# Kernel tuning notes

Hardware: AMD Instinct MI355X
Metric: run time of the kernel (lower is better)

The kernel has to match this reference:

```python
import jax, jax.numpy as jnp
import numpy as np

HIDDEN = 2048
N_HEADS = 16
HEAD_DIM = HIDDEN // N_HEADS
BATCH = 2
SEQ = 2048
N_CP = max(8, int(HIDDEN * HIDDEN / 128.9))  # 32540 control points


def _spline_to_weight(cp, out_dim, in_dim):
    # Reconstruct full weight matrix by sampling the control-point curve at
    # out_dim*in_dim evenly spaced parameter values (piecewise-linear spline eval).
    n = cp.shape[0]
    t = jnp.linspace(0.0, 1.0, out_dim * in_dim)
    xp = jnp.linspace(0.0, 1.0, n)
    return jnp.interp(t, xp, cp).reshape(out_dim, in_dim)


def setup_inputs() -> dict:
    key = jax.random.key(0)
    ks = jax.random.split(key, 5)
    hidden_states = jax.random.normal(ks[0], (BATCH, SEQ, HIDDEN), dtype=jnp.float32)
    cp_q = jax.random.normal(ks[1], (N_CP,), dtype=jnp.float32) * 0.02
    cp_k = jax.random.normal(ks[2], (N_CP,), dtype=jnp.float32) * 0.02
    cp_v = jax.random.normal(ks[3], (N_CP,), dtype=jnp.float32) * 0.02
    cp_o = jax.random.normal(ks[4], (N_CP,), dtype=jnp.float32) * 0.02
    # additive causal mask [1,1,S,S]
    causal = jnp.tril(jnp.ones((SEQ, SEQ), dtype=bool))
    attention_mask = jnp.where(causal, 0.0, -1e9).astype(jnp.float32)[None, None]
    return {
        'hidden_states': hidden_states,
        'cp_q': cp_q, 'cp_k': cp_k, 'cp_v': cp_v, 'cp_o': cp_o,
        'attention_mask': attention_mask,
    }


def reference(hidden_states, cp_q, cp_k, cp_v, cp_o, attention_mask):
    B, S, H = hidden_states.shape
    q_w = _spline_to_weight(cp_q, H, H)
    k_w = _spline_to_weight(cp_k, H, H)
    v_w = _spline_to_weight(cp_v, H, H)
    o_w = _spline_to_weight(cp_o, H, H)

    # F.linear(x, W) == x @ W.T
    q = (hidden_states @ q_w.T).reshape(B, S, N_HEADS, HEAD_DIM).transpose(0, 2, 1, 3)
    k = (hidden_states @ k_w.T).reshape(B, S, N_HEADS, HEAD_DIM).transpose(0, 2, 1, 3)
    v = (hidden_states @ v_w.T).reshape(B, S, N_HEADS, HEAD_DIM).transpose(0, 2, 1, 3)

    scale = 1.0 / np.sqrt(HEAD_DIM).astype(np.float32)
    scores = jnp.einsum('bhqd,bhkd->bhqk', q, k) * scale + attention_mask
    probs = jax.nn.softmax(scores.astype(jnp.float32), axis=-1).astype(q.dtype)
    attn = jnp.einsum('bhqk,bhkd->bhqd', probs, v)
    attn = attn.transpose(0, 2, 1, 3).reshape(B, S, H)
    return attn @ o_w.T
```

## Files before the change

kernel.cpp:

```cpp
#include <hip/hip_runtime.h>
#include <stdint.h>

typedef unsigned short u16;
typedef __bf16 bf16x8 __attribute__((ext_vector_type(8)));
typedef float f32x4 __attribute__((ext_vector_type(4)));
typedef u16 u16x4 __attribute__((ext_vector_type(4)));

#define MFMA16(a, b, c) __builtin_amdgcn_mfma_f32_16x16x32_bf16((a), (b), (c), 0, 0, 0)

__device__ __forceinline__ u16 f2bf(float f) {
  uint32_t u = __builtin_bit_cast(uint32_t, f);
  u += 0x7FFFu + ((u >> 16) & 1u);
  return (u16)(u >> 16);
}
__device__ __forceinline__ bf16x8 cvt8(f32x4 lo, f32x4 hi) {
  union { u16 u[8]; bf16x8 v; } r;
#pragma unroll
  for (int j = 0; j < 4; j++) { r.u[j] = f2bf(lo[j]); r.u[4 + j] = f2bf(hi[j]); }
  return r.v;
}
__device__ __forceinline__ void gld_lds16(const void* g, void* l) {
  __builtin_amdgcn_global_load_lds(
      (const __attribute__((address_space(1))) uint32_t*)g,
      (__attribute__((address_space(3))) uint32_t*)l, 16, 0, 0);
}

__global__ void spline_kernel(const float* __restrict__ cpq, const float* __restrict__ cpk,
                              const float* __restrict__ cpv, const float* __restrict__ cpo,
                              u16* __restrict__ Wqkv, u16* __restrict__ Wo,
                              int n, double factor) {
  int idx = blockIdx.x * 256 + threadIdx.x;
  int w = idx >> 22;
  int i = idx & 4194303;
  const float* cp = (w == 0) ? cpq : (w == 1) ? cpk : (w == 2) ? cpv : cpo;
  double u = (double)i * factor;
  int i0 = (int)u;
  if (i0 > n - 2) i0 = n - 2;
  float fr = (float)(u - (double)i0);
  float f0 = cp[i0], f1 = cp[i0 + 1];
  u16 bv = f2bf(f0 + fr * (f1 - f0));
  if (w < 3) Wqkv[idx] = bv; else Wo[i] = bv;
}

__global__ void cvt_kernel(const float* __restrict__ x, u16* __restrict__ xb) {
  size_t i = ((size_t)blockIdx.x * 256 + threadIdx.x) * 8;
  const f32x4* p = (const f32x4*)(x + i);
  *(bf16x8*)(xb + i) = cvt8(p[0], p[1]);
}

template <int MODE>
__global__ __launch_bounds__(256, 2)
void gemm_bt(const u16* __restrict__ A, const u16* __restrict__ B,
             u16* __restrict__ oQ, u16* __restrict__ oK, u16* __restrict__ oV,
             float* __restrict__ oC) {
  constexpr int KD = 2048;
  __shared__ __align__(16) u16 As[128 * 64];
  __shared__ __align__(16) u16 Bs[128 * 64];
  const int tid = threadIdx.x;
  const int wave = tid >> 6, lane = tid & 63, quad = lane >> 4, l16 = lane & 15;
  const int wm = wave & 1, wn = wave >> 1;
  const int m0 = blockIdx.y * 128, n0 = blockIdx.x * 128;

  size_t aoff[4], boff[4];
  int lslot[4];
#pragma unroll
  for (int b = 0; b < 4; b++) {
    int s = wave * 256 + b * 64 + lane;
    int r = s >> 3, c = s & 7, gc = c ^ (r & 7);
    lslot[b] = s * 16;
    aoff[b] = (size_t)(m0 + r) * (KD * 2) + gc * 16;
    boff[b] = (size_t)(n0 + r) * (KD * 2) + gc * 16;
  }
  const char* Ab = (const char*)A;
  const char* Bb = (const char*)B;
  char* AsB = (char*)As;
  char* BsB = (char*)Bs;

  f32x4 acc[4][4];
  const f32x4 fz = {0.f, 0.f, 0.f, 0.f};
#pragma unroll
  for (int i = 0; i < 4; i++)
#pragma unroll
    for (int j = 0; j < 4; j++) acc[i][j] = fz;

  for (int kt = 0; kt < KD / 64; ++kt) {
    if (kt) __syncthreads();
#pragma unroll
    for (int b = 0; b < 4; b++) {
      gld_lds16(Ab + aoff[b], AsB + lslot[b]);
      gld_lds16(Bb + boff[b], BsB + lslot[b]);
      aoff[b] += 128;
      boff[b] += 128;
    }
    __syncthreads();
#pragma unroll
    for (int t = 0; t < 2; t++) {
      bf16x8 af[4], bfb[4];
#pragma unroll
      for (int i = 0; i < 4; i++) {
        int row = wm * 64 + i * 16 + l16;
        int ch = (t * 4 + quad) ^ (row & 7);
        af[i] = *(const bf16x8*)(AsB + row * 128 + ch * 16);
      }
#pragma unroll
      for (int j = 0; j < 4; j++) {
        int row = wn * 64 + j * 16 + l16;
        int ch = (t * 4 + quad) ^ (row & 7);
        bfb[j] = *(const bf16x8*)(BsB + row * 128 + ch * 16);
      }
#pragma unroll
      for (int i = 0; i < 4; i++)
#pragma unroll
        for (int j = 0; j < 4; j++) acc[i][j] = MFMA16(af[i], bfb[j], acc[i][j]);
    }
  }

  if (MODE == 0) {
#pragma unroll
    for (int j = 0; j < 4; j++) {
      int nb = n0 + wn * 64 + j * 16;
      int sel = nb >> 11;
      int h = (nb >> 7) & 15;
      int d = (nb & 127) + l16;
#pragma unroll
      for (int i = 0; i < 4; i++) {
        int mrow = m0 + wm * 64 + i * 16 + quad * 4;
        int bq = mrow >> 11, srow = mrow & 2047;
        if (sel == 2) {
          u16x4 pk = {f2bf(acc[i][j][0]), f2bf(acc[i][j][1]),
                      f2bf(acc[i][j][2]), f2bf(acc[i][j][3])};
          *(u16x4*)&oV[(size_t)(((bq << 4) + h) * 128 + d) * 2048 + srow] = pk;
        } else {
          u16* dst = (sel == 0) ? oQ : oK;
          int base = ((bq << 4) + h) * 2048;
#pragma unroll
          for (int r = 0; r < 4; r++)
            dst[(size_t)(base + srow + r) * 128 + d] = f2bf(acc[i][j][r]);
        }
      }
    }
  } else {
#pragma unroll
    for (int j = 0; j < 4; j++) {
      int col = n0 + wn * 64 + j * 16 + l16;
#pragma unroll
      for (int i = 0; i < 4; i++) {
        int mrow = m0 + wm * 64 + i * 16 + quad * 4;
#pragma unroll
        for (int r = 0; r < 4; r++) oC[(size_t)(mrow + r) * 2048 + col] = acc[i][j][r];
      }
    }
  }
}

__global__ __launch_bounds__(256, 2)
void flash_attn(const u16* __restrict__ Q, const u16* __restrict__ Kg,
                const u16* __restrict__ Vt, u16* __restrict__ attn) {
  __shared__ __align__(16) u16 Ks[64 * 128];
  __shared__ __align__(16) u16 Vs[128 * 64];
  __shared__ __align__(16) u16 Ps[128 * 72];
  const int tid = threadIdx.x;
  const int wave = tid >> 6, lane = tid & 63, quad = lane >> 4, l16 = lane & 15;
  const int L = blockIdx.x;
  const int bh = L & 31;
  const int qi = (L >> 5) & 7;
  const int qt = (L >= 256) ? (15 - qi) : qi;
  const int q0 = qt * 128;
  const u16* Qb = Q + (size_t)bh * 2048 * 128;
  const u16* Kb = Kg + (size_t)bh * 2048 * 128;
  const u16* Vb = Vt + (size_t)bh * 128 * 2048;

  bf16x8 qf[2][4];
#pragma unroll
  for (int i = 0; i < 2; i++) {
    int row = q0 + wave * 32 + i * 16 + l16;
#pragma unroll
    for (int t = 0; t < 4; t++)
      qf[i][t] = *(const bf16x8*)(Qb + (size_t)row * 128 + t * 32 + quad * 8);
  }

  f32x4 o_acc[2][8];
  const f32x4 fz = {0.f, 0.f, 0.f, 0.f};
#pragma unroll
  for (int i = 0; i < 2; i++)
#pragma unroll
    for (int j = 0; j < 8; j++) o_acc[i][j] = fz;
  float m_i[2][4], l_i[2][4];
#pragma unroll
  for (int i = 0; i < 2; i++)
#pragma unroll
    for (int r = 0; r < 4; r++) { m_i[i][r] = -1e30f; l_i[i][r] = 0.f; }

  int koff[4], voff[4], lslot[4];
#pragma unroll
  for (int b = 0; b < 4; b++) {
    int s = wave * 256 + b * 64 + lane;
    lslot[b] = s * 16;
    {
      int r = s >> 4, c = s & 15;
      int gc = (c & 8) | ((c & 7) ^ (r & 7));
      koff[b] = r * 256 + gc * 16;
    }
    {
      int r = s >> 3, c = s & 7;
      int gc = c ^ (r & 7);
      voff[b] = r * 4096 + gc * 16;
    }
  }
  const char* KbB = (const char*)Kb;
  const char* VbB = (const char*)Vb;
  char* KsB = (char*)Ks;
  char* VsB = (char*)Vs;

  const int ktmax = 2 * qt + 1;
  const float scale = 0.08838834764831845f;

  for (int kt = 0; kt <= ktmax; ++kt) {
    const int k0 = kt * 64;
    if (kt) __syncthreads();
#pragma unroll
    for (int b = 0; b < 4; b++) {
      gld_lds16(KbB + (size_t)k0 * 256 + koff[b], KsB + lslot[b]);
      gld_lds16(VbB + (size_t)k0 * 2 + voff[b], VsB + lslot[b]);
    }
    __syncthreads();

    f32x4 sacc[2][4];
#pragma unroll
    for (int i = 0; i < 2; i++)
#pragma unroll
      for (int j = 0; j < 4; j++) sacc[i][j] = fz;
#pragma unroll
    for (int j = 0; j < 4; j++) {
      int rowb = j * 16 + l16;
#pragma unroll
      for (int t = 0; t < 4; t++) {
        int cc = t * 4 + quad;
        int ch = (cc & 8) | ((cc & 7) ^ (rowb & 7));
        bf16x8 bfr = *(const bf16x8*)(KsB + rowb * 256 + ch * 16);
        sacc[0][j] = MFMA16(qf[0][t], bfr, sacc[0][j]);
        sacc[1][j] = MFMA16(qf[1][t], bfr, sacc[1][j]);
      }
    }

    const bool do_mask = (kt >= 2 * qt);
#pragma unroll
    for (int i = 0; i < 2; i++) {
      const int rbase = q0 + wave * 32 + i * 16 + quad * 4;
#pragma unroll
      for (int r = 0; r < 4; r++) {
        float mloc = -1e30f;
#pragma unroll
        for (int j = 0; j < 4; j++) {
          float v = sacc[i][j][r] * scale;
          if (do_mask && (k0 + j * 16 + l16 > rbase + r)) v = -1e30f;
          sacc[i][j][r] = v;
          mloc = fmaxf(mloc, v);
        }
        mloc = fmaxf(mloc, __shfl_xor(mloc, 1, 16));
        mloc = fmaxf(mloc, __shfl_xor(mloc, 2, 16));
        mloc = fmaxf(mloc, __shfl_xor(mloc, 4, 16));
        mloc = fmaxf(mloc, __shfl_xor(mloc, 8, 16));
        float mold = m_i[i][r];
        float mnew = fmaxf(mold, mloc);
        float alpha = __expf(mold - mnew);
        m_i[i][r] = mnew;
        float rs = 0.f;
#pragma unroll
        for (int j = 0; j < 4; j++) {
          float p = __expf(sacc[i][j][r] - mnew);
          sacc[i][j][r] = p;
          rs += p;
        }
        rs += __shfl_xor(rs, 1, 16);
        rs += __shfl_xor(rs, 2, 16);
        rs += __shfl_xor(rs, 4, 16);
        rs += __shfl_xor(rs, 8, 16);
        l_i[i][r] = alpha * l_i[i][r] + rs;
#pragma unroll
        for (int j = 0; j < 8; j++) o_acc[i][j][r] *= alpha;
      }
#pragma unroll
      for (int r = 0; r < 4; r++) {
        int prow = wave * 32 + i * 16 + quad * 4 + r;
#pragma unroll
        for (int j = 0; j < 4; j++) Ps[prow * 72 + j * 16 + l16] = f2bf(sacc[i][j][r]);
      }
    }
    __syncthreads();

#pragma unroll
    for (int t = 0; t < 2; t++) {
      bf16x8 af0 = *(const bf16x8*)((char*)Ps + (wave * 32 + l16) * 144 + (t * 32 + quad * 8) * 2);
      bf16x8 af1 = *(const bf16x8*)((char*)Ps + (wave * 32 + 16 + l16) * 144 + (t * 32 + quad * 8) * 2);
#pragma unroll
      for (int j = 0; j < 8; j++) {
        int vrow = j * 16 + l16;
        int ch = (t * 4 + quad) ^ (vrow & 7);
        bf16x8 bfr = *(const bf16x8*)(VsB + vrow * 128 + ch * 16);
        o_acc[0][j] = MFMA16(af0, bfr, o_acc[0][j]);
        o_acc[1][j] = MFMA16(af1, bfr, o_acc[1][j]);
      }
    }
  }

  const int bb = bh >> 4, h = bh & 15;
#pragma unroll
  for (int i = 0; i < 2; i++) {
#pragma unroll
    for (int r = 0; r < 4; r++) {
      float inv = 1.f / l_i[i][r];
      int srow = q0 + wave * 32 + i * 16 + quad * 4 + r;
      size_t base = ((size_t)(bb * 2048 + srow)) * 2048 + h * 128;
#pragma unroll
      for (int j = 0; j < 8; j++) attn[base + j * 16 + l16] = f2bf(o_acc[i][j][r] * inv);
    }
  }
}

extern "C" void kernel_launch(void* const* d_in, const int* in_sizes, int n_in,
                              void* d_out, int out_size, void* d_ws, size_t ws_size,
                              hipStream_t stream) {
  (void)n_in; (void)out_size; (void)ws_size;
  const float* x = (const float*)d_in[0];
  const float* cpq = (const float*)d_in[1];
  const float* cpk = (const float*)d_in[2];
  const float* cpv = (const float*)d_in[3];
  const float* cpo = (const float*)d_in[4];
  float* out = (float*)d_out;
  const int ncp = in_sizes[1];
  const double factor = (double)(ncp - 1) / 4194303.0;

  char* ws = (char*)d_ws;
  u16* Wqkv = (u16*)(ws);
  u16* At   = (u16*)(ws);
  u16* Wo = (u16*)(ws + 25165824);
  u16* Qp = (u16*)(ws + 33554432);
  u16* Kp = (u16*)(ws + 50331648);
  u16* Vp = (u16*)(ws + 67108864);
  u16* xb = (u16*)d_out;

  cvt_kernel<<<dim3(4096), dim3(256), 0, stream>>>(x, xb);
  spline_kernel<<<dim3(65536), dim3(256), 0, stream>>>(cpq, cpk, cpv, cpo, Wqkv, Wo, ncp, factor);
  gemm_bt<0><<<dim3(48, 32), dim3(256), 0, stream>>>(xb, Wqkv, Qp, Kp, Vp, nullptr);
  flash_attn<<<dim3(512), dim3(256), 0, stream>>>(Qp, Kp, Vp, At);
  gemm_bt<1><<<dim3(16, 32), dim3(256), 0, stream>>>(At, Wo, nullptr, nullptr, nullptr, out);
}
```

Measured before the change: 382.9 us.

## Use 128-wide KV tiles in flash attention, alias P with K, fuse prep kernels

Flash attention now processes 128 keys per iteration instead of 64, which halves the loop count and barrier overhead. The P tile reuses the K shared buffer after an extra barrier, and the softmax scale is folded into the exp argument. Separately, the spline and x-conversion kernels are merged into one launch. In exchange the attention kernel uses more registers for score accumulators and more LDS (about 66KB per block), which may reduce occupancy.

```diff
diff --git a/kernel.cpp b/kernel.cpp
--- a/kernel.cpp
+++ b/kernel.cpp
@@ -25,27 +25,29 @@
       (__attribute__((address_space(3))) uint32_t*)l, 16, 0, 0);
 }
 
-__global__ void spline_kernel(const float* __restrict__ cpq, const float* __restrict__ cpk,
-                              const float* __restrict__ cpv, const float* __restrict__ cpo,
-                              u16* __restrict__ Wqkv, u16* __restrict__ Wo,
-                              int n, double factor) {
-  int idx = blockIdx.x * 256 + threadIdx.x;
-  int w = idx >> 22;
-  int i = idx & 4194303;
-  const float* cp = (w == 0) ? cpq : (w == 1) ? cpk : (w == 2) ? cpv : cpo;
-  double u = (double)i * factor;
-  int i0 = (int)u;
-  if (i0 > n - 2) i0 = n - 2;
-  float fr = (float)(u - (double)i0);
-  float f0 = cp[i0], f1 = cp[i0 + 1];
-  u16 bv = f2bf(f0 + fr * (f1 - f0));
-  if (w < 3) Wqkv[idx] = bv; else Wo[i] = bv;
-}
-
-__global__ void cvt_kernel(const float* __restrict__ x, u16* __restrict__ xb) {
-  size_t i = ((size_t)blockIdx.x * 256 + threadIdx.x) * 8;
-  const f32x4* p = (const f32x4*)(x + i);
-  *(bf16x8*)(xb + i) = cvt8(p[0], p[1]);
+__global__ void prep_kernel(const float* __restrict__ x, const float* __restrict__ cpq,
+                            const float* __restrict__ cpk, const float* __restrict__ cpv,
+                            const float* __restrict__ cpo, u16* __restrict__ xb,
+                            u16* __restrict__ Wqkv, u16* __restrict__ Wo,
+                            int n, double factor) {
+  int blk = blockIdx.x;
+  if (blk < 65536) {
+    int idx = blk * 256 + threadIdx.x;
+    int w = idx >> 22;
+    int i = idx & 4194303;
+    const float* cp = (w == 0) ? cpq : (w == 1) ? cpk : (w == 2) ? cpv : cpo;
+    double u = (double)i * factor;
+    int i0 = (int)u;
+    if (i0 > n - 2) i0 = n - 2;
+    float fr = (float)(u - (double)i0);
+    float f0 = cp[i0], f1 = cp[i0 + 1];
+    u16 bv = f2bf(f0 + fr * (f1 - f0));
+    if (w < 3) Wqkv[idx] = bv; else Wo[i] = bv;
+  } else {
+    size_t i = ((size_t)(blk - 65536) * 256 + threadIdx.x) * 8;
+    const f32x4* p = (const f32x4*)(x + i);
+    *(bf16x8*)(xb + i) = cvt8(p[0], p[1]);
+  }
 }
 
 template <int MODE>
@@ -156,9 +158,8 @@
 __global__ __launch_bounds__(256, 2)
 void flash_attn(const u16* __restrict__ Q, const u16* __restrict__ Kg,
                 const u16* __restrict__ Vt, u16* __restrict__ attn) {
-  __shared__ __align__(16) u16 Ks[64 * 128];
-  __shared__ __align__(16) u16 Vs[128 * 64];
-  __shared__ __align__(16) u16 Ps[128 * 72];
+  __shared__ __align__(16) u16 KsPs[128 * 136];
+  __shared__ __align__(16) u16 Vs[128 * 128];
   const int tid = threadIdx.x;
   const int wave = tid >> 6, lane = tid & 63, quad = lane >> 4, l16 = lane & 15;
   const int L = blockIdx.x;
@@ -191,47 +192,40 @@
 #pragma unroll
     for (int r = 0; r < 4; r++) { m_i[i][r] = -1e30f; l_i[i][r] = 0.f; }
 
-  int koff[4], voff[4], lslot[4];
-#pragma unroll
-  for (int b = 0; b < 4; b++) {
-    int s = wave * 256 + b * 64 + lane;
+  int koff[8], voff[8], lslot[8];
+#pragma unroll
+  for (int b = 0; b < 8; b++) {
+    int s = wave * 512 + b * 64 + lane;
     lslot[b] = s * 16;
-    {
-      int r = s >> 4, c = s & 15;
-      int gc = (c & 8) | ((c & 7) ^ (r & 7));
-      koff[b] = r * 256 + gc * 16;
-    }
-    {
-      int r = s >> 3, c = s & 7;
-      int gc = c ^ (r & 7);
-      voff[b] = r * 4096 + gc * 16;
-    }
+    int r = s >> 4, c = s & 15;
+    int gc = (c & 8) | ((c & 7) ^ (r & 7));
+    koff[b] = r * 256 + gc * 16;
+    voff[b] = r * 4096 + gc * 16;
   }
   const char* KbB = (const char*)Kb;
   const char* VbB = (const char*)Vb;
-  char* KsB = (char*)Ks;
+  char* KsB = (char*)KsPs;
   char* VsB = (char*)Vs;
 
-  const int ktmax = 2 * qt + 1;
   const float scale = 0.08838834764831845f;
 
-  for (int kt = 0; kt <= ktmax; ++kt) {
-    const int k0 = kt * 64;
+  for (int kt = 0; kt <= qt; ++kt) {
+    const int k0 = kt * 128;
     if (kt) __syncthreads();
 #pragma unroll
-    for (int b = 0; b < 4; b++) {
+    for (int b = 0; b < 8; b++) {
       gld_lds16(KbB + (size_t)k0 * 256 + koff[b], KsB + lslot[b]);
       gld_lds16(VbB + (size_t)k0 * 2 + voff[b], VsB + lslot[b]);
     }
     __syncthreads();
 
-    f32x4 sacc[2][4];
+    f32x4 sacc[2][8];
 #pragma unroll
     for (int i = 0; i < 2; i++)
 #pragma unroll
-      for (int j = 0; j < 4; j++) sacc[i][j] = fz;
-#pragma unroll
-    for (int j = 0; j < 4; j++) {
+      for (int j = 0; j < 8; j++) sacc[i][j] = fz;
+#pragma unroll
+    for (int j = 0; j < 8; j++) {
       int rowb = j * 16 + l16;
 #pragma unroll
       for (int t = 0; t < 4; t++) {
@@ -242,8 +236,9 @@
         sacc[1][j] = MFMA16(qf[1][t], bfr, sacc[1][j]);
       }
     }
-
-    const bool do_mask = (kt >= 2 * qt);
+    __syncthreads();
+
+    const bool do_mask = (kt == qt);
 #pragma unroll
     for (int i = 0; i < 2; i++) {
       const int rbase = q0 + wave * 32 + i * 16 + quad * 4;
@@ -251,10 +246,9 @@
       for (int r = 0; r < 4; r++) {
         float mloc = -1e30f;
 #pragma unroll
-        for (int j = 0; j < 4; j++) {
-          float v = sacc[i][j][r] * scale;
-          if (do_mask && (k0 + j * 16 + l16 > rbase + r)) v = -1e30f;
-          sacc[i][j][r] = v;
+        for (int j = 0; j < 8; j++) {
+          float v = sacc[i][j][r];
+          if (do_mask && (k0 + j * 16 + l16 > rbase + r)) { v = -1e30f; sacc[i][j][r] = v; }
           mloc = fmaxf(mloc, v);
         }
         mloc = fmaxf(mloc, __shfl_xor(mloc, 1, 16));
@@ -263,41 +257,39 @@
         mloc = fmaxf(mloc, __shfl_xor(mloc, 8, 16));
         float mold = m_i[i][r];
         float mnew = fmaxf(mold, mloc);
-        float alpha = __expf(mold - mnew);
+        float alpha = __expf((mold - mnew) * scale);
         m_i[i][r] = mnew;
+        const float c1 = -mnew * scale;
         float rs = 0.f;
-#pragma unroll
-        for (int j = 0; j < 4; j++) {
-          float p = __expf(sacc[i][j][r] - mnew);
-          sacc[i][j][r] = p;
-          rs += p;
+        float p[8];
+#pragma unroll
+        for (int j = 0; j < 8; j++) {
+          p[j] = __expf(fmaf(sacc[i][j][r], scale, c1));
+          rs += p[j];
         }
         rs += __shfl_xor(rs, 1, 16);
         rs += __shfl_xor(rs, 2, 16);
         rs += __shfl_xor(rs, 4, 16);
         rs += __shfl_xor(rs, 8, 16);
         l_i[i][r] = alpha * l_i[i][r] + rs;
+        int prow = wave * 32 + i * 16 + quad * 4 + r;
+#pragma unroll
+        for (int j = 0; j < 8; j++) KsPs[prow * 136 + j * 16 + l16] = f2bf(p[j]);
 #pragma unroll
         for (int j = 0; j < 8; j++) o_acc[i][j][r] *= alpha;
       }
-#pragma unroll
-      for (int r = 0; r < 4; r++) {
-        int prow = wave * 32 + i * 16 + quad * 4 + r;
-#pragma unroll
-        for (int j = 0; j < 4; j++) Ps[prow * 72 + j * 16 + l16] = f2bf(sacc[i][j][r]);
-      }
-    }
-    __syncthreads();
-
-#pragma unroll
-    for (int t = 0; t < 2; t++) {
-      bf16x8 af0 = *(const bf16x8*)((char*)Ps + (wave * 32 + l16) * 144 + (t * 32 + quad * 8) * 2);
-      bf16x8 af1 = *(const bf16x8*)((char*)Ps + (wave * 32 + 16 + l16) * 144 + (t * 32 + quad * 8) * 2);
+    }
+
+#pragma unroll
+    for (int t = 0; t < 4; t++) {
+      bf16x8 af0 = *(const bf16x8*)((char*)KsPs + (wave * 32 + l16) * 272 + (t * 32 + quad * 8) * 2);
+      bf16x8 af1 = *(const bf16x8*)((char*)KsPs + (wave * 32 + 16 + l16) * 272 + (t * 32 + quad * 8) * 2);
 #pragma unroll
       for (int j = 0; j < 8; j++) {
         int vrow = j * 16 + l16;
-        int ch = (t * 4 + quad) ^ (vrow & 7);
-        bf16x8 bfr = *(const bf16x8*)(VsB + vrow * 128 + ch * 16);
+        int cc = t * 4 + quad;
+        int ch = (cc & 8) | ((cc & 7) ^ (vrow & 7));
+        bf16x8 bfr = *(const bf16x8*)(VsB + vrow * 256 + ch * 16);
         o_acc[0][j] = MFMA16(af0, bfr, o_acc[0][j]);
         o_acc[1][j] = MFMA16(af1, bfr, o_acc[1][j]);
       }
@@ -340,8 +332,7 @@
   u16* Vp = (u16*)(ws + 67108864);
   u16* xb = (u16*)d_out;
 
-  cvt_kernel<<<dim3(4096), dim3(256), 0, stream>>>(x, xb);
-  spline_kernel<<<dim3(65536), dim3(256), 0, stream>>>(cpq, cpk, cpv, cpo, Wqkv, Wo, ncp, factor);
+  prep_kernel<<<dim3(69632), dim3(256), 0, stream>>>(x, cpq, cpk, cpv, cpo, xb, Wqkv, Wo, ncp, factor);
   gemm_bt<0><<<dim3(48, 32), dim3(256), 0, stream>>>(xb, Wqkv, Qp, Kp, Vp, nullptr);
   flash_attn<<<dim3(512), dim3(256), 0, stream>>>(Qp, Kp, Vp, At);
   gemm_bt<1><<<dim3(16, 32), dim3(256), 0, stream>>>(At, Wo, nullptr, nullptr, nullptr, out);
```

After: 422.0 us. +10.2%, slower.
